# Kernel tuning notes

Measured on AMD Instinct MI355X. Metric: run time of the kernel, lower is better.

## Reference

```python
import jax, jax.numpy as jnp
import numpy as np

GRID_LENGTH = 8.0
GRID_SIZE = 32
ATOM_TYPE = 6


def generate_grid(grid_length, grid_size):
    # matches torch generate_grid: x varies slowest, z fastest -> meshgrid 'ij'
    half = grid_length / 2.0
    ticks = jnp.linspace(-half, half, grid_size, dtype=jnp.float32)
    gx, gy, gz = jnp.meshgrid(ticks, ticks, ticks, indexing='ij')
    return jnp.stack([gx, gy, gz], axis=-1)  # (G,G,G,3)


def setup_inputs() -> dict:
    key = jax.random.key(0)
    k1, k2 = jax.random.split(key)
    distance_vector = jax.random.normal(k1, (4, 32, 16, 3), dtype=jnp.float32) * 2.0
    atomic_numbers = jax.random.randint(k2, (32, 16), 0, 10, dtype=jnp.int64 if jax.config.read('jax_enable_x64') else jnp.int32)
    sigma = jnp.ones((1,), dtype=jnp.float32)
    return {"distance_vector": distance_vector, "atomic_numbers": atomic_numbers, "sigma": sigma}


def reference(distance_vector, atomic_numbers, sigma):
    # distance_vector: (B, A, N, 3); atomic_numbers: (A, N); sigma: (1,)
    grid = generate_grid(GRID_LENGTH, GRID_SIZE)  # (G,G,G,3)
    # diff: (B, A, N, G, G, G, 3)
    diff = grid[None, None, None] - distance_vector[:, :, :, None, None, None, :]
    sq = jnp.sum(diff * diff, axis=-1)  # ||grid - dv||^2, (B,A,N,G,G,G)
    coeff = -0.5 / (sigma[0] * sigma[0])
    box = jnp.exp(coeff * sq)
    mask = (atomic_numbers == ATOM_TYPE).astype(box.dtype)  # (A,N)
    # masked sum over neighbor axis N -> (B, A, G, G, G)
    out = jnp.sum(box * mask[None, :, :, None, None, None], axis=2)
    return out
```

## Files before the change

kernel.cpp:

```cpp
#include <hip/hip_runtime.h>
#include <hip/hip_bf16.h>

#define G 32
#define NNBR 16
#define ATOM_TYPE 6

__global__ __launch_bounds__(256) void voxel_kernel(
    const float* __restrict__ dv,
    const int*   __restrict__ an,
    const float* __restrict__ sigma,
    float*       __restrict__ out)
{
    const int ba    = blockIdx.x;
    const int a     = ba & 31;
    const int islab = blockIdx.y;
    const int tid   = threadIdx.x;

    __shared__ __align__(16) float sEx[NNBR][G];
    __shared__ __align__(16) float sEy[NNBR][G];
    __shared__ __align__(16) float sEz[NNBR][G];
    __shared__ float sDv[NNBR * 3];
    __shared__ int   sIdx[NNBR];
    __shared__ int   sM;

    if (tid < NNBR * 3) sDv[tid] = dv[(size_t)ba * (NNBR * 3) + tid];

    int flag = 0;
    if (tid < NNBR) flag = (an[a * NNBR + tid] == ATOM_TYPE) ? 1 : 0;
    unsigned long long mask = __ballot(flag);
    if (flag) {
        int pos = __popcll(mask & ((1ull << tid) - 1ull));
        sIdx[pos] = tid;
    }
    if (tid == 0) sM = (int)__popcll(mask);
    __syncthreads();

    const int   M     = sM;
    const float s     = sigma[0];
    const float coeff = -0.5f / (s * s);
    const float step  = 8.0f / 31.0f;

    for (int idx = tid; idx < M * G; idx += 256) {
        const int m = idx >> 5;
        const int i = idx & 31;
        const int n = sIdx[m];
        const float t  = -4.0f + (float)i * step;
        const float dx = t - sDv[3 * n + 0];
        const float dy = t - sDv[3 * n + 1];
        const float dz = t - sDv[3 * n + 2];
        sEx[m][i] = __expf(coeff * dx * dx);
        sEy[m][i] = __expf(coeff * dy * dy);
        sEz[m][i] = __expf(coeff * dz * dz);
    }
    __syncthreads();

    const int j  = tid >> 3;
    const int k0 = (tid & 7) * 4;
    const int i0 = islab * 4;

    float4 acc0 = {0.f, 0.f, 0.f, 0.f};
    float4 acc1 = acc0, acc2 = acc0, acc3 = acc0;

    for (int m = 0; m < M; ++m) {
        const float  ey = sEy[m][j];
        const float4 ez = *(const float4*)&sEz[m][k0];
        const float4 ex = *(const float4*)&sEx[m][i0];
        const float p0 = ex.x * ey, p1 = ex.y * ey, p2 = ex.z * ey, p3 = ex.w * ey;
        acc0.x += p0 * ez.x; acc0.y += p0 * ez.y; acc0.z += p0 * ez.z; acc0.w += p0 * ez.w;
        acc1.x += p1 * ez.x; acc1.y += p1 * ez.y; acc1.z += p1 * ez.z; acc1.w += p1 * ez.w;
        acc2.x += p2 * ez.x; acc2.y += p2 * ez.y; acc2.z += p2 * ez.z; acc2.w += p2 * ez.w;
        acc3.x += p3 * ez.x; acc3.y += p3 * ez.y; acc3.z += p3 * ez.z; acc3.w += p3 * ez.w;
    }

    float4* out4 = (float4*)(out + (size_t)ba * (G * G * G) + (size_t)islab * 4096);
    out4[0 * 256 + tid] = acc0;
    out4[1 * 256 + tid] = acc1;
    out4[2 * 256 + tid] = acc2;
    out4[3 * 256 + tid] = acc3;
}

extern "C" void kernel_launch(void* const* d_in, const int* in_sizes, int n_in,
                              void* d_out, int out_size, void* d_ws, size_t ws_size,
                              hipStream_t stream) {
    const float* dv    = (const float*)d_in[0];
    const int*   an    = (const int*)d_in[1];
    const float* sigma = (const float*)d_in[2];
    float*       out   = (float*)d_out;

    dim3 grid(4 * 32, 8);
    dim3 block(256);
    voxel_kernel<<<grid, block, 0, stream>>>(dv, an, sigma, out);
}
```

Baseline: 63.80 us.

## Assign one x-slice per block and fold Ex*Ey into a precomputed plane table

Launches one block per (batch-atom, x index) instead of per 4-x slab, giving four times as many blocks, each writing a single 4 KB x-plane. Each block precomputes a combined exp of the x and y terms per neighbor and y index, so the inner loop does one multiply-add per output instead of a multiply followed by a multiply-add. The cost is that the per-neighbor setup (sDv load, ballot, exp tables) is repeated four times as often across blocks, and each thread now holds one float4 accumulator instead of four.

Result: no change. 63.99 us (+0.3%).

```diff
diff --git a/kernel.cpp b/kernel.cpp
--- a/kernel.cpp
+++ b/kernel.cpp
@@ -11,13 +11,12 @@
     const float* __restrict__ sigma,
     float*       __restrict__ out)
 {
-    const int ba    = blockIdx.x;
-    const int a     = ba & 31;
-    const int islab = blockIdx.y;
-    const int tid   = threadIdx.x;
+    const int ba  = blockIdx.x;
+    const int a   = ba & 31;
+    const int i   = blockIdx.y;
+    const int tid = threadIdx.x;
 
-    __shared__ __align__(16) float sEx[NNBR][G];
-    __shared__ __align__(16) float sEy[NNBR][G];
+    __shared__ __align__(16) float sP [NNBR][G];
     __shared__ __align__(16) float sEz[NNBR][G];
     __shared__ float sDv[NNBR * 3];
     __shared__ int   sIdx[NNBR];
@@ -39,44 +38,36 @@
     const float s     = sigma[0];
     const float coeff = -0.5f / (s * s);
     const float step  = 8.0f / 31.0f;
+    const float ti    = -4.0f + (float)i * step;
 
     for (int idx = tid; idx < M * G; idx += 256) {
         const int m = idx >> 5;
-        const int i = idx & 31;
+        const int j = idx & 31;
         const int n = sIdx[m];
-        const float t  = -4.0f + (float)i * step;
-        const float dx = t - sDv[3 * n + 0];
-        const float dy = t - sDv[3 * n + 1];
-        const float dz = t - sDv[3 * n + 2];
-        sEx[m][i] = __expf(coeff * dx * dx);
-        sEy[m][i] = __expf(coeff * dy * dy);
-        sEz[m][i] = __expf(coeff * dz * dz);
+        const float tj  = -4.0f + (float)j * step;
+        const float dxv = ti - sDv[3 * n + 0];
+        const float dyv = tj - sDv[3 * n + 1];
+        const float dzv = tj - sDv[3 * n + 2];
+        sP [m][j] = __expf(coeff * (dxv * dxv + dyv * dyv));
+        sEz[m][j] = __expf(coeff * (dzv * dzv));
     }
     __syncthreads();
 
     const int j  = tid >> 3;
-    const int k0 = (tid & 7) * 4;
-    const int i0 = islab * 4;
+    const int k0 = (tid & 7) << 2;
 
-    float4 acc0 = {0.f, 0.f, 0.f, 0.f};
-    float4 acc1 = acc0, acc2 = acc0, acc3 = acc0;
-
+    float4 acc = {0.f, 0.f, 0.f, 0.f};
     for (int m = 0; m < M; ++m) {
-        const float  ey = sEy[m][j];
+        const float  p  = sP[m][j];
         const float4 ez = *(const float4*)&sEz[m][k0];
-        const float4 ex = *(const float4*)&sEx[m][i0];
-        const float p0 = ex.x * ey, p1 = ex.y * ey, p2 = ex.z * ey, p3 = ex.w * ey;
-        acc0.x += p0 * ez.x; acc0.y += p0 * ez.y; acc0.z += p0 * ez.z; acc0.w += p0 * ez.w;
-        acc1.x += p1 * ez.x; acc1.y += p1 * ez.y; acc1.z += p1 * ez.z; acc1.w += p1 * ez.w;
-        acc2.x += p2 * ez.x; acc2.y += p2 * ez.y; acc2.z += p2 * ez.z; acc2.w += p2 * ez.w;
-        acc3.x += p3 * ez.x; acc3.y += p3 * ez.y; acc3.z += p3 * ez.z; acc3.w += p3 * ez.w;
+        acc.x += p * ez.x;
+        acc.y += p * ez.y;
+        acc.z += p * ez.z;
+        acc.w += p * ez.w;
     }
 
-    float4* out4 = (float4*)(out + (size_t)ba * (G * G * G) + (size_t)islab * 4096);
-    out4[0 * 256 + tid] = acc0;
-    out4[1 * 256 + tid] = acc1;
-    out4[2 * 256 + tid] = acc2;
-    out4[3 * 256 + tid] = acc3;
+    float4* out4 = (float4*)(out + ((size_t)ba * G + i) * (G * G));
+    out4[tid] = acc;
 }
 
 extern "C" void kernel_launch(void* const* d_in, const int* in_sizes, int n_in,
@@ -87,7 +78,7 @@
     const float* sigma = (const float*)d_in[2];
     float*       out   = (float*)d_out;
 
-    dim3 grid(4 * 32, 8);
+    dim3 grid(4 * 32, G);
     dim3 block(256);
     voxel_kernel<<<grid, block, 0, stream>>>(dv, an, sigma, out);
 }
```
